# Kernel tuning notes

Hardware: AMD Instinct MI355X
Metric: run time of the kernel (lower is better)

## Reference

```python
import jax, jax.numpy as jnp
import numpy as np

B, D, H = 262144, 64, 64

def setup_inputs() -> dict:
    key = jax.random.key(0)
    ks = jax.random.split(key, 9)
    t = jax.random.uniform(ks[0], (1,), dtype=jnp.float32)
    z = jax.random.normal(ks[1], (B, D), dtype=jnp.float32)
    # Rademacher noise: randint in {0,1} -> {-1,+1}
    e = (jax.random.randint(ks[2], (B, D), 0, 2).astype(jnp.float32) * 2.0 - 1.0)
    def lin(k, fan_in, fan_out):
        bound = 1.0 / np.sqrt(fan_in)
        kw, kb = jax.random.split(k)
        W = jax.random.uniform(kw, (fan_out, fan_in), minval=-bound, maxval=bound, dtype=jnp.float32)
        b = jax.random.uniform(kb, (fan_out,), minval=-bound, maxval=bound, dtype=jnp.float32)
        return W, b
    W0, b0 = lin(ks[3], D + 1, H)
    W1, b1 = lin(ks[4], H + 1, H)
    W2, b2 = lin(ks[5], H + 1, D)
    return {"t": t, "z": z, "e": e, "W0": W0, "b0": b0, "W1": W1, "b1": b1, "W2": W2, "b2": b2}

def _mlp(t, z, params):
    # per-layer time concat: h <- act(Linear([t, h]))
    h = z
    n = len(params)
    tcol = jnp.broadcast_to(t.reshape(1, 1), (z.shape[0], 1)).astype(z.dtype)
    for i, (W, b) in enumerate(params):
        tz = jnp.concatenate([tcol, h], axis=1)          # [B, dim+1]
        h = tz @ W.T + b                                  # [B, out]
        if i < n - 1:
            h = jax.nn.relu(h)
    return h

def reference(t, z, e, W0, b0, W1, b1, W2, b2):
    params = [(W0, b0), (W1, b1), (W2, b2)]
    f = lambda zz: _mlp(t, zz, params)
    z_dot, vjp_fn = jax.vjp(f, z)                         # e^T (df/dz) via VJP
    e_dfdz = vjp_fn(e)[0]                                 # [B, D]
    div = jnp.sum(e_dfdz * e, axis=1, keepdims=True)      # Hutchinson trace estimate [B,1]
    return (z_dot, -div)
```

## Files before the change

kernel.cpp:

```cpp
#include <hip/hip_runtime.h>

typedef unsigned short u16;
typedef unsigned int   u32;
typedef __attribute__((ext_vector_type(4))) float  f32x4;
typedef __attribute__((ext_vector_type(8))) __bf16 bf16x8;

#define RPB   1024
#define ITERS 16
#define HSTRF 68
#define HSTR  72
#define SMEM_BYTES 100096

__device__ __forceinline__ u32 pkbf(float a, float b){
  u16 ua = __builtin_bit_cast(u16, (__bf16)a);
  u16 ub = __builtin_bit_cast(u16, (__bf16)b);
  return (u32)ua | ((u32)ub << 16);
}
__device__ __forceinline__ u32 pk2(__bf16 a, __bf16 b){
  return (u32)__builtin_bit_cast(u16, a) | ((u32)__builtin_bit_cast(u16, b) << 16);
}
__device__ __forceinline__ bf16x8 ldfrag(const u16* base, int idx){
  return __builtin_bit_cast(bf16x8, *(const uint4*)(base + (size_t)idx * 8));
}
__device__ __forceinline__ bf16x8 cvt8(float4 a, float4 b){
  uint4 u;
  u.x = pkbf(a.x, a.y); u.y = pkbf(a.z, a.w);
  u.z = pkbf(b.x, b.y); u.w = pkbf(b.z, b.w);
  return __builtin_bit_cast(bf16x8, u);
}
__device__ __forceinline__ f32x4 mfma16(bf16x8 a, bf16x8 b, f32x4 c){
  return __builtin_amdgcn_mfma_f32_16x16x32_bf16(a, b, c, 0, 0, 0);
}
__device__ __forceinline__ void split8(float4 a, float4 b, bf16x8* out){
  float x[8] = {a.x, a.y, a.z, a.w, b.x, b.y, b.z, b.w};
  bf16x8 l0, l1, l2;
  #pragma unroll
  for (int j = 0; j < 8; ++j){
    float v = x[j];
    __bf16 p0 = (__bf16)v; float r = v - (float)p0;
    __bf16 p1 = (__bf16)r; r = r - (float)p1;
    __bf16 p2 = (__bf16)r;
    l0[j] = p0; l1[j] = p1; l2[j] = p2;
  }
  out[0] = l0; out[1] = l1; out[2] = l2;
}
__device__ __forceinline__ f32x4 hp_tile(const u16* w0, const u16* w1, const u16* w2,
                                         int mt, int lane, const bf16x8* B0, const bf16x8* B1){
  f32x4 c = {0.f, 0.f, 0.f, 0.f};
  const int f0 = (mt*2+0)*64 + lane, f1 = (mt*2+1)*64 + lane;
  bf16x8 A0 = ldfrag(w0, f0), A1 = ldfrag(w1, f0), A2 = ldfrag(w2, f0);
  c = mfma16(A0, B0[0], c); c = mfma16(A0, B0[1], c); c = mfma16(A1, B0[0], c);
  c = mfma16(A0, B0[2], c); c = mfma16(A1, B0[1], c); c = mfma16(A2, B0[0], c);
  A0 = ldfrag(w0, f1); A1 = ldfrag(w1, f1); A2 = ldfrag(w2, f1);
  c = mfma16(A0, B1[0], c); c = mfma16(A0, B1[1], c); c = mfma16(A1, B1[0], c);
  c = mfma16(A0, B1[2], c); c = mfma16(A1, B1[1], c); c = mfma16(A2, B1[0], c);
  return c;
}

__global__ __launch_bounds__(256, 1) void ode_fused(
    const float* __restrict__ tptr, const float* __restrict__ z, const float* __restrict__ e,
    const float* __restrict__ W0p, const float* __restrict__ b0p,
    const float* __restrict__ W1p, const float* __restrict__ b1p,
    const float* __restrict__ W2p, const float* __restrict__ b2p,
    float* __restrict__ out, long long Btot)
{
  extern __shared__ __align__(16) char smem[];
  u16*   wf3  = (u16*)smem;
  u16*   wf2  = wf3 + 6*4096;
  u16*   wb   = wf2 + 4096;
  float* bias = (float*)(wb + 3*4096);
  float* hbuf = bias + 192;

  const int tid = threadIdx.x;
  const float tf = tptr[0];
  const float* Ws[3] = {W0p, W1p, W2p};
  const float* bs[3] = {b0p, b1p, b2p};

  for (int L = 0; L < 3; ++L){
    const float* W = Ws[L];
    for (int eidx = tid; eidx < 512; eidx += 256){
      const int l = eidx & 63, km = eidx >> 6;
      const int mt = km >> 1, kc = km & 1;
      const int n15 = l & 15, q = l >> 4;
      {
        const float* p = W + (mt*16 + n15)*65 + 1 + kc*32 + q*8;
        if (L < 2){
          uint4 u0, u1, u2;
          u32* d0 = (u32*)&u0; u32* d1 = (u32*)&u1; u32* d2 = (u32*)&u2;
          #pragma unroll
          for (int h = 0; h < 4; ++h){
            __bf16 a0, a1, a2, b0_, b1_, b2_;
            float v = p[2*h];
            a0 = (__bf16)v; float r = v - (float)a0;
            a1 = (__bf16)r; r = r - (float)a1; a2 = (__bf16)r;
            v = p[2*h+1];
            b0_ = (__bf16)v; r = v - (float)b0_;
            b1_ = (__bf16)r; r = r - (float)b1_; b2_ = (__bf16)r;
            d0[h] = pk2(a0, b0_); d1[h] = pk2(a1, b1_); d2[h] = pk2(a2, b2_);
          }
          *(uint4*)(&wf3[(L*3+0)*4096 + eidx*8]) = u0;
          *(uint4*)(&wf3[(L*3+1)*4096 + eidx*8]) = u1;
          *(uint4*)(&wf3[(L*3+2)*4096 + eidx*8]) = u2;
        } else {
          uint4 u;
          u.x = pkbf(p[0], p[1]); u.y = pkbf(p[2], p[3]);
          u.z = pkbf(p[4], p[5]); u.w = pkbf(p[6], p[7]);
          *(uint4*)(&wf2[eidx*8]) = u;
        }
      }
      {
        const float* p = W + (kc*32 + q*8)*65 + mt*16 + n15 + 1;
        uint4 u;
        u.x = pkbf(p[0],   p[65]);  u.y = pkbf(p[130], p[195]);
        u.z = pkbf(p[260], p[325]); u.w = pkbf(p[390], p[455]);
        *(uint4*)(&wb[L*4096 + eidx*8]) = u;
      }
    }
  }
  if (tid < 192){
    const int L = tid >> 6, m = tid & 63;
    bias[L*64 + m] = bs[L][m] + tf * Ws[L][m*65];
  }
  __syncthreads();

  const int wave = tid >> 6, lane = tid & 63;
  const int n = lane & 15, q = lane >> 4;
  float* hbF = hbuf + wave*16*HSTRF;
  float* hwF = hbF + n*HSTRF + q*4;
  const float* hrF = hbF + n*HSTRF + q*8;
  u16* hbU = (u16*)hbF;
  u16* hwU = hbU + n*HSTR + q*4;
  const u16* hrU = hbU + n*HSTR + q*8;

  for (int it = 0; it < ITERS; ++it){
    const int r0 = blockIdx.x*RPB + (it*4 + wave)*16;
    const size_t row = (size_t)(r0 + n);

    const float4* zr = (const float4*)(z + row*64);
    bf16x8 zB0[3], zB1[3];
    split8(zr[2*q],     zr[2*q + 1], zB0);
    split8(zr[8 + 2*q], zr[9 + 2*q], zB1);

    f32x4 h0[4];
    #pragma unroll
    for (int mt = 0; mt < 4; ++mt){
      f32x4 c = hp_tile(&wf3[0], &wf3[4096], &wf3[2*4096], mt, lane, zB0, zB1);
      const f32x4 bv = *(const f32x4*)(&bias[0*64 + mt*16 + q*4]);
      #pragma unroll
      for (int r = 0; r < 4; ++r){
        float v = c[r] + bv[r];
        h0[mt][r] = v > 0.f ? v : 0.f;
      }
    }
    #pragma unroll
    for (int mt = 0; mt < 4; ++mt)
      *(float4*)(hwF + mt*16) = __builtin_bit_cast(float4, h0[mt]);
    __syncthreads();
    bf16x8 h0B0[3], h0B1[3];
    split8(*(const float4*)(hrF),      *(const float4*)(hrF + 4),  h0B0);
    split8(*(const float4*)(hrF + 32), *(const float4*)(hrF + 36), h0B1);

    f32x4 h1[4];
    #pragma unroll
    for (int mt = 0; mt < 4; ++mt){
      f32x4 c = hp_tile(&wf3[3*4096], &wf3[4*4096], &wf3[5*4096], mt, lane, h0B0, h0B1);
      const f32x4 bv = *(const f32x4*)(&bias[1*64 + mt*16 + q*4]);
      #pragma unroll
      for (int r = 0; r < 4; ++r){
        float v = c[r] + bv[r];
        h1[mt][r] = v > 0.f ? v : 0.f;
      }
    }
    __syncthreads();
    #pragma unroll
    for (int mt = 0; mt < 4; ++mt){
      uint2 w; w.x = pkbf(h1[mt][0], h1[mt][1]); w.y = pkbf(h1[mt][2], h1[mt][3]);
      *(uint2*)(hwU + mt*16) = w;
    }
    __syncthreads();
    const bf16x8 h1b0 = __builtin_bit_cast(bf16x8, *(const uint4*)(hrU));
    const bf16x8 h1b1 = __builtin_bit_cast(bf16x8, *(const uint4*)(hrU + 32));

    #pragma unroll
    for (int mt = 0; mt < 4; ++mt){
      f32x4 c = {0.f, 0.f, 0.f, 0.f};
      c = mfma16(ldfrag(wf2, (mt*2+0)*64 + lane), h1b0, c);
      c = mfma16(ldfrag(wf2, (mt*2+1)*64 + lane), h1b1, c);
      const f32x4 bv = *(const f32x4*)(&bias[2*64 + mt*16 + q*4]);
      float4 w;
      w.x = c[0] + bv[0]; w.y = c[1] + bv[1];
      w.z = c[2] + bv[2]; w.w = c[3] + bv[3];
      *(float4*)(out + row*64 + mt*16 + q*4) = w;
    }

    const float4* er = (const float4*)(e + row*64);
    const bf16x8 eb0 = cvt8(er[2*q],     er[2*q + 1]);
    const bf16x8 eb1 = cvt8(er[8 + 2*q], er[9 + 2*q]);

    f32x4 g1[4];
    #pragma unroll
    for (int mt = 0; mt < 4; ++mt){
      f32x4 c = {0.f, 0.f, 0.f, 0.f};
      c = mfma16(ldfrag(&wb[2*4096], (mt*2+0)*64 + lane), eb0, c);
      c = mfma16(ldfrag(&wb[2*4096], (mt*2+1)*64 + lane), eb1, c);
      #pragma unroll
      for (int r = 0; r < 4; ++r)
        g1[mt][r] = (h1[mt][r] > 0.f) ? c[r] : 0.f;
    }
    #pragma unroll
    for (int mt = 0; mt < 4; ++mt){
      uint2 w; w.x = pkbf(g1[mt][0], g1[mt][1]); w.y = pkbf(g1[mt][2], g1[mt][3]);
      *(uint2*)(hwU + mt*16) = w;
    }
    __syncthreads();
    const bf16x8 g1b0 = __builtin_bit_cast(bf16x8, *(const uint4*)(hrU));
    const bf16x8 g1b1 = __builtin_bit_cast(bf16x8, *(const uint4*)(hrU + 32));

    f32x4 g0[4];
    #pragma unroll
    for (int mt = 0; mt < 4; ++mt){
      f32x4 c = {0.f, 0.f, 0.f, 0.f};
      c = mfma16(ldfrag(&wb[1*4096], (mt*2+0)*64 + lane), g1b0, c);
      c = mfma16(ldfrag(&wb[1*4096], (mt*2+1)*64 + lane), g1b1, c);
      #pragma unroll
      for (int r = 0; r < 4; ++r)
        g0[mt][r] = (h0[mt][r] > 0.f) ? c[r] : 0.f;
    }
    #pragma unroll
    for (int mt = 0; mt < 4; ++mt){
      uint2 w; w.x = pkbf(g0[mt][0], g0[mt][1]); w.y = pkbf(g0[mt][2], g0[mt][3]);
      *(uint2*)(hwU + mt*16) = w;
    }
    __syncthreads();
    const bf16x8 g0b0 = __builtin_bit_cast(bf16x8, *(const uint4*)(hrU));
    const bf16x8 g0b1 = __builtin_bit_cast(bf16x8, *(const uint4*)(hrU + 32));

    float s = 0.f;
    #pragma unroll
    for (int mt = 0; mt < 4; ++mt){
      f32x4 c = {0.f, 0.f, 0.f, 0.f};
      c = mfma16(ldfrag(&wb[0], (mt*2+0)*64 + lane), g0b0, c);
      c = mfma16(ldfrag(&wb[0], (mt*2+1)*64 + lane), g0b1, c);
      const float4 ec = *(const float4*)(e + row*64 + mt*16 + q*4);
      s += c[0]*ec.x + c[1]*ec.y + c[2]*ec.z + c[3]*ec.w;
    }
    s += __shfl_xor(s, 16, 64);
    s += __shfl_xor(s, 32, 64);
    if (lane < 16)
      out[(size_t)Btot*64 + r0 + lane] = -s;
  }
}

extern "C" void kernel_launch(void* const* d_in, const int* in_sizes, int n_in,
                              void* d_out, int out_size, void* d_ws, size_t ws_size,
                              hipStream_t stream){
  const float* t  = (const float*)d_in[0];
  const float* z  = (const float*)d_in[1];
  const float* e  = (const float*)d_in[2];
  const float* W0 = (const float*)d_in[3];
  const float* b0 = (const float*)d_in[4];
  const float* W1 = (const float*)d_in[5];
  const float* b1 = (const float*)d_in[6];
  const float* W2 = (const float*)d_in[7];
  const float* b2 = (const float*)d_in[8];
  float* out = (float*)d_out;
  const long long B = (long long)in_sizes[1] / 64;
  const int grid = (int)(B / RPB);
  ode_fused<<<grid, 256, SMEM_BYTES, stream>>>(t, z, e, W0, b0, W1, b1, W2, b2, out, B);
}
```

Measured before the change: 228.8 us.

## Replace LDS transposes with shuffles, process two row tiles per wave, refactor divergence

Removes the shared-memory staging buffer and all __syncthreads in the per-row loop, transposing MFMA outputs into B-operand layout with cross-lane shuffles instead. Each wave now handles two 16-row tiles so weight fragments loaded from LDS are reused twice. The last backward layer is replaced by computing W0·e directly and dotting it with the masked W1ᵀ·g1 term, which drops one transpose stage. Block size and LDS use shrink so two blocks can share a CU, at the cost of more registers, many shuffle instructions and a different bf16 rounding path for the divergence.

```diff
diff --git a/kernel.cpp b/kernel.cpp
--- a/kernel.cpp
+++ b/kernel.cpp
@@ -5,11 +5,9 @@
 typedef __attribute__((ext_vector_type(4))) float  f32x4;
 typedef __attribute__((ext_vector_type(8))) __bf16 bf16x8;
 
-#define RPB   1024
-#define ITERS 16
-#define HSTRF 68
-#define HSTR  72
-#define SMEM_BYTES 100096
+#define RPB   512
+#define ITERS 4
+#define SMEM_BYTES 74496
 
 __device__ __forceinline__ u32 pkbf(float a, float b){
   u16 ua = __builtin_bit_cast(u16, (__bf16)a);
@@ -44,20 +42,70 @@
   }
   out[0] = l0; out[1] = l1; out[2] = l2;
 }
-__device__ __forceinline__ f32x4 hp_tile(const u16* w0, const u16* w1, const u16* w2,
-                                         int mt, int lane, const bf16x8* B0, const bf16x8* B1){
-  f32x4 c = {0.f, 0.f, 0.f, 0.f};
-  const int f0 = (mt*2+0)*64 + lane, f1 = (mt*2+1)*64 + lane;
-  bf16x8 A0 = ldfrag(w0, f0), A1 = ldfrag(w1, f0), A2 = ldfrag(w2, f0);
-  c = mfma16(A0, B0[0], c); c = mfma16(A0, B0[1], c); c = mfma16(A1, B0[0], c);
-  c = mfma16(A0, B0[2], c); c = mfma16(A1, B0[1], c); c = mfma16(A2, B0[0], c);
-  A0 = ldfrag(w0, f1); A1 = ldfrag(w1, f1); A2 = ldfrag(w2, f1);
-  c = mfma16(A0, B1[0], c); c = mfma16(A0, B1[1], c); c = mfma16(A1, B1[0], c);
-  c = mfma16(A0, B1[2], c); c = mfma16(A1, B1[1], c); c = mfma16(A2, B1[0], c);
-  return c;
-}
-
-__global__ __launch_bounds__(256, 1) void ode_fused(
+__device__ __forceinline__ float4 shflf4(f32x4 v, int src){
+  float4 r;
+  r.x = __shfl(v[0], src, 64); r.y = __shfl(v[1], src, 64);
+  r.z = __shfl(v[2], src, 64); r.w = __shfl(v[3], src, 64);
+  return r;
+}
+__device__ __forceinline__ uint2 shflu2(uint2 v, int src){
+  uint2 r;
+  r.x = (u32)__shfl((int)v.x, src, 64);
+  r.y = (u32)__shfl((int)v.y, src, 64);
+  return r;
+}
+__device__ __forceinline__ void xpose_f32(const f32x4 h[4], int srcA, int srcB, bool hi,
+                                          bf16x8* B0, bf16x8* B1){
+  float4 Fa0 = shflf4(h[0], srcA), Fb0 = shflf4(h[0], srcB);
+  float4 Fa1 = shflf4(h[1], srcA), Fb1 = shflf4(h[1], srcB);
+  float4 Fa2 = shflf4(h[2], srcA), Fb2 = shflf4(h[2], srcB);
+  float4 Fa3 = shflf4(h[3], srcA), Fb3 = shflf4(h[3], srcB);
+  float4 lo0 = hi ? Fa1 : Fa0, hi0 = hi ? Fb1 : Fb0;
+  float4 lo1 = hi ? Fa3 : Fa2, hi1 = hi ? Fb3 : Fb2;
+  split8(lo0, hi0, B0);
+  split8(lo1, hi1, B1);
+}
+__device__ __forceinline__ void xpose_bf(const uint2 p[4], int srcA, int srcB, bool hi,
+                                         bf16x8* B0, bf16x8* B1){
+  uint2 Pa0 = shflu2(p[0], srcA), Pb0 = shflu2(p[0], srcB);
+  uint2 Pa1 = shflu2(p[1], srcA), Pb1 = shflu2(p[1], srcB);
+  uint2 Pa2 = shflu2(p[2], srcA), Pb2 = shflu2(p[2], srcB);
+  uint2 Pa3 = shflu2(p[3], srcA), Pb3 = shflu2(p[3], srcB);
+  uint2 a0 = hi ? Pa1 : Pa0, b0 = hi ? Pb1 : Pb0;
+  uint2 a1 = hi ? Pa3 : Pa2, b1 = hi ? Pb3 : Pb2;
+  uint4 u0; u0.x = a0.x; u0.y = a0.y; u0.z = b0.x; u0.w = b0.y;
+  uint4 u1; u1.x = a1.x; u1.y = a1.y; u1.z = b1.x; u1.w = b1.y;
+  *B0 = __builtin_bit_cast(bf16x8, u0);
+  *B1 = __builtin_bit_cast(bf16x8, u1);
+}
+__device__ __forceinline__ void hp_layer(const u16* w0, const u16* w1, const u16* w2,
+    int lane, const bf16x8 Bv[2][2][3], f32x4 hout[2][4]){
+  #pragma unroll
+  for (int mt = 0; mt < 4; ++mt){
+    const int f0 = (mt*2+0)*64 + lane, f1 = (mt*2+1)*64 + lane;
+    bf16x8 A00 = ldfrag(w0, f0), A01 = ldfrag(w1, f0), A02 = ldfrag(w2, f0);
+    bf16x8 A10 = ldfrag(w0, f1), A11 = ldfrag(w1, f1), A12 = ldfrag(w2, f1);
+    #pragma unroll
+    for (int c = 0; c < 2; ++c){
+      f32x4 a = {0.f, 0.f, 0.f, 0.f};
+      a = mfma16(A00, Bv[c][0][0], a);
+      a = mfma16(A00, Bv[c][0][1], a);
+      a = mfma16(A01, Bv[c][0][0], a);
+      a = mfma16(A00, Bv[c][0][2], a);
+      a = mfma16(A01, Bv[c][0][1], a);
+      a = mfma16(A02, Bv[c][0][0], a);
+      a = mfma16(A10, Bv[c][1][0], a);
+      a = mfma16(A10, Bv[c][1][1], a);
+      a = mfma16(A11, Bv[c][1][0], a);
+      a = mfma16(A10, Bv[c][1][2], a);
+      a = mfma16(A11, Bv[c][1][1], a);
+      a = mfma16(A12, Bv[c][1][0], a);
+      hout[c][mt] = a;
+    }
+  }
+}
+
+__global__ __launch_bounds__(256, 2) void ode_fused(
     const float* __restrict__ tptr, const float* __restrict__ z, const float* __restrict__ e,
     const float* __restrict__ W0p, const float* __restrict__ b0p,
     const float* __restrict__ W1p, const float* __restrict__ b1p,
@@ -68,8 +116,7 @@
   u16*   wf3  = (u16*)smem;
   u16*   wf2  = wf3 + 6*4096;
   u16*   wb   = wf2 + 4096;
-  float* bias = (float*)(wb + 3*4096);
-  float* hbuf = bias + 192;
+  float* bias = (float*)(wb + 2*4096);
 
   const int tid = threadIdx.x;
   const float tf = tptr[0];
@@ -89,14 +136,14 @@
           u32* d0 = (u32*)&u0; u32* d1 = (u32*)&u1; u32* d2 = (u32*)&u2;
           #pragma unroll
           for (int h = 0; h < 4; ++h){
-            __bf16 a0, a1, a2, b0_, b1_, b2_;
+            __bf16 a0, a1, a2, c0, c1, c2;
             float v = p[2*h];
             a0 = (__bf16)v; float r = v - (float)a0;
             a1 = (__bf16)r; r = r - (float)a1; a2 = (__bf16)r;
             v = p[2*h+1];
-            b0_ = (__bf16)v; r = v - (float)b0_;
-            b1_ = (__bf16)r; r = r - (float)b1_; b2_ = (__bf16)r;
-            d0[h] = pk2(a0, b0_); d1[h] = pk2(a1, b1_); d2[h] = pk2(a2, b2_);
+            c0 = (__bf16)v; r = v - (float)c0;
+            c1 = (__bf16)r; r = r - (float)c1; c2 = (__bf16)r;
+            d0[h] = pk2(a0, c0); d1[h] = pk2(a1, c1); d2[h] = pk2(a2, c2);
           }
           *(uint4*)(&wf3[(L*3+0)*4096 + eidx*8]) = u0;
           *(uint4*)(&wf3[(L*3+1)*4096 + eidx*8]) = u1;
@@ -108,12 +155,12 @@
           *(uint4*)(&wf2[eidx*8]) = u;
         }
       }
-      {
+      if (L >= 1){
         const float* p = W + (kc*32 + q*8)*65 + mt*16 + n15 + 1;
         uint4 u;
         u.x = pkbf(p[0],   p[65]);  u.y = pkbf(p[130], p[195]);
         u.z = pkbf(p[260], p[325]); u.w = pkbf(p[390], p[455]);
-        *(uint4*)(&wb[L*4096 + eidx*8]) = u;
+        *(uint4*)(&wb[(L-1)*4096 + eidx*8]) = u;
       }
     }
   }
@@ -125,129 +172,140 @@
 
   const int wave = tid >> 6, lane = tid & 63;
   const int n = lane & 15, q = lane >> 4;
-  float* hbF = hbuf + wave*16*HSTRF;
-  float* hwF = hbF + n*HSTRF + q*4;
-  const float* hrF = hbF + n*HSTRF + q*8;
-  u16* hbU = (u16*)hbF;
-  u16* hwU = hbU + n*HSTR + q*4;
-  const u16* hrU = hbU + n*HSTR + q*8;
+  const int srcA = n + 16*(2*(q & 1));
+  const int srcB = srcA + 16;
+  const bool hi = (q & 2) != 0;
 
   for (int it = 0; it < ITERS; ++it){
-    const int r0 = blockIdx.x*RPB + (it*4 + wave)*16;
-    const size_t row = (size_t)(r0 + n);
-
-    const float4* zr = (const float4*)(z + row*64);
-    bf16x8 zB0[3], zB1[3];
-    split8(zr[2*q],     zr[2*q + 1], zB0);
-    split8(zr[8 + 2*q], zr[9 + 2*q], zB1);
-
-    f32x4 h0[4];
+    const int r0 = blockIdx.x*RPB + (it*4 + wave)*32;
+    const size_t row0 = (size_t)(r0 + n);
+    const size_t row1 = (size_t)(r0 + 16 + n);
+
+    bf16x8 zB[2][2][3];
+    {
+      const float4* zr = (const float4*)(z + row0*64);
+      split8(zr[2*q], zr[2*q+1], &zB[0][0][0]);
+      split8(zr[8+2*q], zr[9+2*q], &zB[0][1][0]);
+      const float4* zr1 = (const float4*)(z + row1*64);
+      split8(zr1[2*q], zr1[2*q+1], &zB[1][0][0]);
+      split8(zr1[8+2*q], zr1[9+2*q], &zB[1][1][0]);
+    }
+
+    f32x4 h0[2][4];
+    hp_layer(wf3 + 0*4096, wf3 + 1*4096, wf3 + 2*4096, lane, zB, h0);
+    #pragma unroll
+    for (int c = 0; c < 2; ++c)
+      #pragma unroll
+      for (int mt = 0; mt < 4; ++mt){
+        const f32x4 bv = *(const f32x4*)(&bias[0*64 + mt*16 + q*4]);
+        #pragma unroll
+        for (int r = 0; r < 4; ++r){
+          float v = h0[c][mt][r] + bv[r];
+          h0[c][mt][r] = v > 0.f ? v : 0.f;
+        }
+      }
+    bf16x8 h0B[2][2][3];
+    xpose_f32(h0[0], srcA, srcB, hi, &h0B[0][0][0], &h0B[0][1][0]);
+    xpose_f32(h0[1], srcA, srcB, hi, &h0B[1][0][0], &h0B[1][1][0]);
+
+    f32x4 h1[2][4];
+    hp_layer(wf3 + 3*4096, wf3 + 4*4096, wf3 + 5*4096, lane, h0B, h1);
+    uint2 ph[2][4];
+    #pragma unroll
+    for (int c = 0; c < 2; ++c)
+      #pragma unroll
+      for (int mt = 0; mt < 4; ++mt){
+        const f32x4 bv = *(const f32x4*)(&bias[1*64 + mt*16 + q*4]);
+        #pragma unroll
+        for (int r = 0; r < 4; ++r){
+          float v = h1[c][mt][r] + bv[r];
+          h1[c][mt][r] = v > 0.f ? v : 0.f;
+        }
+        ph[c][mt].x = pkbf(h1[c][mt][0], h1[c][mt][1]);
+        ph[c][mt].y = pkbf(h1[c][mt][2], h1[c][mt][3]);
+      }
+    bf16x8 h1B[2][2];
+    xpose_bf(ph[0], srcA, srcB, hi, &h1B[0][0], &h1B[0][1]);
+    xpose_bf(ph[1], srcA, srcB, hi, &h1B[1][0], &h1B[1][1]);
+
     #pragma unroll
     for (int mt = 0; mt < 4; ++mt){
-      f32x4 c = hp_tile(&wf3[0], &wf3[4096], &wf3[2*4096], mt, lane, zB0, zB1);
-      const f32x4 bv = *(const f32x4*)(&bias[0*64 + mt*16 + q*4]);
-      #pragma unroll
-      for (int r = 0; r < 4; ++r){
-        float v = c[r] + bv[r];
-        h0[mt][r] = v > 0.f ? v : 0.f;
-      }
-    }
-    #pragma unroll
-    for (int mt = 0; mt < 4; ++mt)
-      *(float4*)(hwF + mt*16) = __builtin_bit_cast(float4, h0[mt]);
-    __syncthreads();
-    bf16x8 h0B0[3], h0B1[3];
-    split8(*(const float4*)(hrF),      *(const float4*)(hrF + 4),  h0B0);
-    split8(*(const float4*)(hrF + 32), *(const float4*)(hrF + 36), h0B1);
-
-    f32x4 h1[4];
+      bf16x8 A0 = ldfrag(wf2, (mt*2+0)*64 + lane);
+      bf16x8 A1 = ldfrag(wf2, (mt*2+1)*64 + lane);
+      const f32x4 bv = *(const f32x4*)(&bias[2*64 + mt*16 + q*4]);
+      #pragma unroll
+      for (int c = 0; c < 2; ++c){
+        f32x4 a = {0.f, 0.f, 0.f, 0.f};
+        a = mfma16(A0, h1B[c][0], a);
+        a = mfma16(A1, h1B[c][1], a);
+        float4 w;
+        w.x = a[0] + bv[0]; w.y = a[1] + bv[1];
+        w.z = a[2] + bv[2]; w.w = a[3] + bv[3];
+        const size_t rr = (c == 0) ? row0 : row1;
+        *(float4*)(out + rr*64 + mt*16 + q*4) = w;
+      }
+    }
+
+    bf16x8 eB[2][2];
+    {
+      const float4* er = (const float4*)(e + row0*64);
+      eB[0][0] = cvt8(er[2*q], er[2*q+1]);
+      eB[0][1] = cvt8(er[8+2*q], er[9+2*q]);
+      const float4* er1 = (const float4*)(e + row1*64);
+      eB[1][0] = cvt8(er1[2*q], er1[2*q+1]);
+      eB[1][1] = cvt8(er1[8+2*q], er1[9+2*q]);
+    }
+
+    uint2 pg[2][4];
     #pragma unroll
     for (int mt = 0; mt < 4; ++mt){
-      f32x4 c = hp_tile(&wf3[3*4096], &wf3[4*4096], &wf3[5*4096], mt, lane, h0B0, h0B1);
-      const f32x4 bv = *(const f32x4*)(&bias[1*64 + mt*16 + q*4]);
-      #pragma unroll
-      for (int r = 0; r < 4; ++r){
-        float v = c[r] + bv[r];
-        h1[mt][r] = v > 0.f ? v : 0.f;
-      }
-    }
-    __syncthreads();
+      bf16x8 A0 = ldfrag(wb + 4096, (mt*2+0)*64 + lane);
+      bf16x8 A1 = ldfrag(wb + 4096, (mt*2+1)*64 + lane);
+      #pragma unroll
+      for (int c = 0; c < 2; ++c){
+        f32x4 a = {0.f, 0.f, 0.f, 0.f};
+        a = mfma16(A0, eB[c][0], a);
+        a = mfma16(A1, eB[c][1], a);
+        float v0 = h1[c][mt][0] > 0.f ? a[0] : 0.f;
+        float v1 = h1[c][mt][1] > 0.f ? a[1] : 0.f;
+        float v2 = h1[c][mt][2] > 0.f ? a[2] : 0.f;
+        float v3 = h1[c][mt][3] > 0.f ? a[3] : 0.f;
+        pg[c][mt].x = pkbf(v0, v1);
+        pg[c][mt].y = pkbf(v2, v3);
+      }
+    }
+    bf16x8 g1B[2][2];
+    xpose_bf(pg[0], srcA, srcB, hi, &g1B[0][0], &g1B[0][1]);
+    xpose_bf(pg[1], srcA, srcB, hi, &g1B[1][0], &g1B[1][1]);
+
+    float s0a = 0.f, s1a = 0.f;
     #pragma unroll
     for (int mt = 0; mt < 4; ++mt){
-      uint2 w; w.x = pkbf(h1[mt][0], h1[mt][1]); w.y = pkbf(h1[mt][2], h1[mt][3]);
-      *(uint2*)(hwU + mt*16) = w;
-    }
-    __syncthreads();
-    const bf16x8 h1b0 = __builtin_bit_cast(bf16x8, *(const uint4*)(hrU));
-    const bf16x8 h1b1 = __builtin_bit_cast(bf16x8, *(const uint4*)(hrU + 32));
-
-    #pragma unroll
-    for (int mt = 0; mt < 4; ++mt){
-      f32x4 c = {0.f, 0.f, 0.f, 0.f};
-      c = mfma16(ldfrag(wf2, (mt*2+0)*64 + lane), h1b0, c);
-      c = mfma16(ldfrag(wf2, (mt*2+1)*64 + lane), h1b1, c);
-      const f32x4 bv = *(const f32x4*)(&bias[2*64 + mt*16 + q*4]);
-      float4 w;
-      w.x = c[0] + bv[0]; w.y = c[1] + bv[1];
-      w.z = c[2] + bv[2]; w.w = c[3] + bv[3];
-      *(float4*)(out + row*64 + mt*16 + q*4) = w;
-    }
-
-    const float4* er = (const float4*)(e + row*64);
-    const bf16x8 eb0 = cvt8(er[2*q],     er[2*q + 1]);
-    const bf16x8 eb1 = cvt8(er[8 + 2*q], er[9 + 2*q]);
-
-    f32x4 g1[4];
-    #pragma unroll
-    for (int mt = 0; mt < 4; ++mt){
-      f32x4 c = {0.f, 0.f, 0.f, 0.f};
-      c = mfma16(ldfrag(&wb[2*4096], (mt*2+0)*64 + lane), eb0, c);
-      c = mfma16(ldfrag(&wb[2*4096], (mt*2+1)*64 + lane), eb1, c);
-      #pragma unroll
-      for (int r = 0; r < 4; ++r)
-        g1[mt][r] = (h1[mt][r] > 0.f) ? c[r] : 0.f;
-    }
-    #pragma unroll
-    for (int mt = 0; mt < 4; ++mt){
-      uint2 w; w.x = pkbf(g1[mt][0], g1[mt][1]); w.y = pkbf(g1[mt][2], g1[mt][3]);
-      *(uint2*)(hwU + mt*16) = w;
-    }
-    __syncthreads();
-    const bf16x8 g1b0 = __builtin_bit_cast(bf16x8, *(const uint4*)(hrU));
-    const bf16x8 g1b1 = __builtin_bit_cast(bf16x8, *(const uint4*)(hrU + 32));
-
-    f32x4 g0[4];
-    #pragma unroll
-    for (int mt = 0; mt < 4; ++mt){
-      f32x4 c = {0.f, 0.f, 0.f, 0.f};
-      c = mfma16(ldfrag(&wb[1*4096], (mt*2+0)*64 + lane), g1b0, c);
-      c = mfma16(ldfrag(&wb[1*4096], (mt*2+1)*64 + lane), g1b1, c);
-      #pragma unroll
-      for (int r = 0; r < 4; ++r)
-        g0[mt][r] = (h0[mt][r] > 0.f) ? c[r] : 0.f;
-    }
-    #pragma unroll
-    for (int mt = 0; mt < 4; ++mt){
-      uint2 w; w.x = pkbf(g0[mt][0], g0[mt][1]); w.y = pkbf(g0[mt][2], g0[mt][3]);
-      *(uint2*)(hwU + mt*16) = w;
-    }
-    __syncthreads();
-    const bf16x8 g0b0 = __builtin_bit_cast(bf16x8, *(const uint4*)(hrU));
-    const bf16x8 g0b1 = __builtin_bit_cast(bf16x8, *(const uint4*)(hrU + 32));
-
-    float s = 0.f;
-    #pragma unroll
-    for (int mt = 0; mt < 4; ++mt){
-      f32x4 c = {0.f, 0.f, 0.f, 0.f};
-      c = mfma16(ldfrag(&wb[0], (mt*2+0)*64 + lane), g0b0, c);
-      c = mfma16(ldfrag(&wb[0], (mt*2+1)*64 + lane), g0b1, c);
-      const float4 ec = *(const float4*)(e + row*64 + mt*16 + q*4);
-      s += c[0]*ec.x + c[1]*ec.y + c[2]*ec.z + c[3]*ec.w;
-    }
-    s += __shfl_xor(s, 16, 64);
-    s += __shfl_xor(s, 32, 64);
-    if (lane < 16)
-      out[(size_t)Btot*64 + r0 + lane] = -s;
+      bf16x8 G0 = ldfrag(wb, (mt*2+0)*64 + lane);
+      bf16x8 G1 = ldfrag(wb, (mt*2+1)*64 + lane);
+      bf16x8 U0 = ldfrag(wf3, (mt*2+0)*64 + lane);
+      bf16x8 U1 = ldfrag(wf3, (mt*2+1)*64 + lane);
+      #pragma unroll
+      for (int c = 0; c < 2; ++c){
+        f32x4 g = {0.f, 0.f, 0.f, 0.f};
+        g = mfma16(G0, g1B[c][0], g);
+        g = mfma16(G1, g1B[c][1], g);
+        f32x4 u = {0.f, 0.f, 0.f, 0.f};
+        u = mfma16(U0, eB[c][0], u);
+        u = mfma16(U1, eB[c][1], u);
+        float acc = 0.f;
+        #pragma unroll
+        for (int r = 0; r < 4; ++r)
+          acc += (h0[c][mt][r] > 0.f) ? g[r]*u[r] : 0.f;
+        if (c == 0) s0a += acc; else s1a += acc;
+      }
+    }
+    s0a += __shfl_xor(s0a, 16, 64); s0a += __shfl_xor(s0a, 32, 64);
+    s1a += __shfl_xor(s1a, 16, 64); s1a += __shfl_xor(s1a, 32, 64);
+    if (lane < 16){
+      out[(size_t)Btot*64 + r0 + n]      = -s0a;
+      out[(size_t)Btot*64 + r0 + 16 + n] = -s1a;
+    }
   }
 }
 
```

Result: slower. 276.5 us (+20.8%).
